# Optimization experiments

Measured on AMD Instinct MI355X. Metric: run time of the kernel, lower is better.

Reference implementation:

```python
import jax, jax.numpy as jnp
import numpy as np
import math

B, C, H, W, M = 8, 256, 128, 128, 7
EPS = 1e-08


def setup_inputs() -> dict:
    key = jax.random.key(0)
    ks = jax.random.split(key, 7)
    x_high = jax.random.normal(ks[0], (B, C, H // 2, W // 2), jnp.float32)
    x_low = jax.random.normal(ks[1], (B, C, H, W), jnp.float32)
    w1 = jax.random.normal(ks[2], (32, M * M), jnp.float32) / np.sqrt(M * M)
    b1 = jnp.zeros((32,), jnp.float32)
    w2 = jax.random.normal(ks[3], (3, 32), jnp.float32) / np.sqrt(32)
    b2 = jnp.zeros((3,), jnp.float32)
    refine_w = jax.random.normal(ks[4], (C, C), jnp.float32) / np.sqrt(C)
    return {"x_high": x_high, "x_low": x_low, "w1": w1, "b1": b1,
            "w2": w2, "b2": b2, "refine_w": refine_w}


def _anisotropic_kernel(params):
    # params: (B,3) -> normalized Gaussian kernels (B, m, m)
    theta = jnp.arctan2(params[:, 0], params[:, 1]) / 2.0 + math.pi / 2.0
    lam1 = jnp.exp(params[:, 2])
    lam2 = 1.0 / (lam1 + EPS)
    coords = jnp.arange(M, dtype=jnp.float32) - (M // 2)  # -3..3
    yy = coords[:, None]  # (m,1) varies along rows (torch meshgrid 'ij')
    xx = coords[None, :]  # (1,m)
    cos_t = jnp.cos(theta)[:, None, None]
    sin_t = jnp.sin(theta)[:, None, None]
    x_rot = xx * cos_t + yy * sin_t          # (B,m,m)
    y_rot = -xx * sin_t + yy * cos_t
    l1 = lam1[:, None, None]
    l2 = lam2[:, None, None]
    k = jnp.exp(-(x_rot ** 2 / (2.0 * l1 ** 2) + y_rot ** 2 / (2.0 * l2 ** 2)))
    return k / (jnp.sum(k, axis=(1, 2), keepdims=True) + EPS)


def _depthwise(x, kern):
    # x: (B,C,H,W), kern: (B,m,m) -> per-sample depthwise conv, kernel shared across C
    k = jnp.repeat(kern, C, axis=0)[:, None, :, :]  # (B*C,1,m,m)
    pad = M // 2
    y = jax.lax.conv_general_dilated(
        x.reshape(1, B * C, H, W), k, (1, 1), [(pad, pad), (pad, pad)],
        dimension_numbers=("NCHW", "OIHW", "NCHW"), feature_group_count=B * C)
    return y.reshape(B, C, H, W)


def reference(x_high, x_low, w1, b1, w2, b2, refine_w):
    # bilinear upsample (align_corners=False == half-pixel, matches jax.image.resize)
    x_high_up = jax.image.resize(x_high, (B, C, H, W), method="bilinear")

    x_f = jnp.fft.fftshift(jnp.fft.fft2(x_low, norm="ortho"), axes=(-2, -1))
    real, imag = jnp.real(x_f), jnp.imag(x_f)
    mag = jnp.abs(x_f)
    mag_weighted = jnp.mean(mag, axis=1, keepdims=True)  # (B,1,H,W)
    h0, w0 = H // 2 - M // 2, W // 2 - M // 2
    mag_center = mag_weighted[:, :, h0:h0 + M, w0:w0 + M]  # (B,1,m,m)

    # param_net: Flatten -> Linear -> ReLU -> Linear
    flat = mag_center.reshape(B, M * M)
    h = jax.nn.relu(flat @ w1.T + b1)
    params = h @ w2.T + b2  # (B,3)

    kern = _anisotropic_kernel(params)
    real_f = _depthwise(real, kern)
    imag_f = _depthwise(imag, kern)

    # 1x1 refine conv (bias-free), shared for real and imag parts
    real_f = jnp.einsum("bchw,oc->bohw", real_f, refine_w)
    imag_f = jnp.einsum("bchw,oc->bohw", imag_f, refine_w)

    out_f = jax.lax.complex(real_f, imag_f)
    out_f = jnp.fft.ifftshift(out_f, axes=(-2, -1))
    x_low_enhanced = jnp.real(jnp.fft.ifft2(out_f, norm="ortho"))
    return x_low_enhanced + x_high_up
```

## Files before the change

### kernel.cpp

```cpp
#include <hip/hip_runtime.h>

typedef __attribute__((ext_vector_type(8))) short bf16x8;
typedef __attribute__((ext_vector_type(4))) float f32x4;
typedef __attribute__((ext_vector_type(4))) int   i32x4;

#define PI_F 3.14159265358979323846f
#define C128 0.0490873852123405f
#define INV_SQRT128 0.0883883476483184f
#define INV128 0.0078125f

#define NB 8
#define NC 256
#define NH 128
#define NW 128
#define IMG 16384
#define NIMG 2048
#define XST 130

#define GH_STRIDE 3200
#define AB_STRIDE 3072

__device__ __forceinline__ unsigned short f2bf(float f){
  unsigned int u = __float_as_uint(f);
  u += 0x7FFFu + ((u >> 16) & 1u);
  return (unsigned short)(u >> 16);
}
__device__ __forceinline__ float bf2f(unsigned short u){
  return __uint_as_float(((unsigned int)u) << 16);
}

__device__ __constant__ int c_pcnt[6] = {1,2,3,3,2,1};
__device__ __constant__ int c_pdp0[6] = {6,5,4,0,0,0};

#define COS1 0.9987954562051724f
#define SIN1 0.0490676743274180f
#define K1CH (2.0f*COS1)

__global__ void __launch_bounds__(256) K1(const float* __restrict__ xlow,
                                          float* __restrict__ GH){
  __shared__ unsigned short xs[128*XST];
  __shared__ float Hlo[4][2][128];
  __shared__ float Hhi[4][2][128];
  __shared__ float Gg [4][2][128];
  __shared__ float twc[128], tws[128];

  const int tid = threadIdx.x;
  const int img = blockIdx.x;
  float* ghb = GH + (size_t)img*GH_STRIDE;

  if (tid < 128){
    float s,c; __sincosf((float)tid*C128, &s, &c);
    twc[tid]=c; tws[tid]=s;
  }
  {
    const float4* xp = (const float4*)(xlow + (size_t)img*IMG);
    #pragma unroll
    for (int k=0; k<16; ++k){
      int e4 = k*256 + tid;
      float4 v = xp[e4];
      int px = e4*4;
      int r = px >> 7, c = px & 127;
      unsigned int pw0 = (unsigned int)f2bf(v.x) | ((unsigned int)f2bf(v.y) << 16);
      unsigned int pw1 = (unsigned int)f2bf(v.z) | ((unsigned int)f2bf(v.w) << 16);
      *(unsigned int*)(&xs[r*XST + c    ]) = pw0;
      *(unsigned int*)(&xs[r*XST + c + 2]) = pw1;
    }
  }
  __syncthreads();

  float A0e=0.f, A0o=0.f;
  float Ce1=0.f,Se1=0.f,Co1=0.f,So1=0.f;
  float Ce2=0.f,Se2=0.f,Co2=0.f,So2=0.f;
  float Ce3=0.f,Se3=0.f,Co3=0.f,So3=0.f;

  if (tid < 128){
    const int r = tid;
    const unsigned short* xr = &xs[r*XST];
    float cp = 1.f, sp = 0.f;
    float cn = COS1, sn = SIN1;
    #pragma unroll 4
    for (int j=0; j<64; ++j){
      unsigned int pk = *(const unsigned int*)(&xr[2*j]);
      float xe = __uint_as_float(pk << 16);
      float xo = __uint_as_float(pk & 0xffff0000u);
      {
        float t2 = cp + cp;
        float c2 = fmaf(t2, cp, -1.f);
        float s2 = t2 * sp;
        float c3 = fmaf(t2, c2, -cp);
        float s3 = fmaf(t2, s2, -sp);
        A0e += xe;
        Ce1 = fmaf(xe, cp, Ce1); Se1 = fmaf(xe, sp, Se1);
        Ce2 = fmaf(xe, c2, Ce2); Se2 = fmaf(xe, s2, Se2);
        Ce3 = fmaf(xe, c3, Ce3); Se3 = fmaf(xe, s3, Se3);
      }
      {
        float t2 = cn + cn;
        float c2 = fmaf(t2, cn, -1.f);
        float s2 = t2 * sn;
        float c3 = fmaf(t2, c2, -cn);
        float s3 = fmaf(t2, s2, -sn);
        A0o += xo;
        Co1 = fmaf(xo, cn, Co1); So1 = fmaf(xo, sn, So1);
        Co2 = fmaf(xo, c2, Co2); So2 = fmaf(xo, s2, So2);
        Co3 = fmaf(xo, c3, Co3); So3 = fmaf(xo, s3, So3);
      }
      float cpn = fmaf(K1CH, cn, -cp);
      float spn = fmaf(K1CH, sn, -sp);
      float cnn = fmaf(K1CH, cpn, -cn);
      float snn = fmaf(K1CH, spn, -sn);
      cp = cpn; sp = spn; cn = cnn; sn = snn;
    }
    Hlo[0][0][r]=A0e+A0o;  Hlo[0][1][r]=0.f;
    Hlo[1][0][r]=Ce1+Co1;  Hlo[1][1][r]=-(Se1+So1);
    Hlo[2][0][r]=Ce2+Co2;  Hlo[2][1][r]=-(Se2+So2);
    Hlo[3][0][r]=Ce3+Co3;  Hlo[3][1][r]=-(Se3+So3);
    Hhi[0][0][r]=Ce3-Co3;  Hhi[0][1][r]=Se3-So3;
    Hhi[1][0][r]=Ce2-Co2;  Hhi[1][1][r]=Se2-So2;
    Hhi[2][0][r]=Ce1-Co1;  Hhi[2][1][r]=Se1-So1;
    Hhi[3][0][r]=A0e-A0o;  Hhi[3][1][r]=0.f;
  } else {
    const int c = tid - 128;
    float cp = 1.f, sp = 0.f;
    float cn = COS1, sn = SIN1;
    #pragma unroll 4
    for (int j=0; j<64; ++j){
      float xe = bf2f(xs[(2*j  )*XST + c]);
      float xo = bf2f(xs[(2*j+1)*XST + c]);
      {
        float t2 = cp + cp;
        float c2 = fmaf(t2, cp, -1.f);
        float s2 = t2 * sp;
        float c3 = fmaf(t2, c2, -cp);
        float s3 = fmaf(t2, s2, -sp);
        A0e += xe;
        Ce1 = fmaf(xe, cp, Ce1); Se1 = fmaf(xe, sp, Se1);
        Ce2 = fmaf(xe, c2, Ce2); Se2 = fmaf(xe, s2, Se2);
        Ce3 = fmaf(xe, c3, Ce3); Se3 = fmaf(xe, s3, Se3);
      }
      {
        float t2 = cn + cn;
        float c2 = fmaf(t2, cn, -1.f);
        float s2 = t2 * sn;
        float c3 = fmaf(t2, c2, -cn);
        float s3 = fmaf(t2, s2, -sn);
        A0o += xo;
        Co1 = fmaf(xo, cn, Co1); So1 = fmaf(xo, sn, So1);
        Co2 = fmaf(xo, c2, Co2); So2 = fmaf(xo, s2, So2);
        Co3 = fmaf(xo, c3, Co3); So3 = fmaf(xo, s3, So3);
      }
      float cpn = fmaf(K1CH, cn, -cp);
      float spn = fmaf(K1CH, sn, -sp);
      float cnn = fmaf(K1CH, cpn, -cn);
      float snn = fmaf(K1CH, spn, -sn);
      cp = cpn; sp = spn; cn = cnn; sn = snn;
    }
    Gg[0][0][c]=Ce3-Co3;  Gg[0][1][c]=Se3-So3;
    Gg[1][0][c]=Ce2-Co2;  Gg[1][1][c]=Se2-So2;
    Gg[2][0][c]=Ce1-Co1;  Gg[2][1][c]=Se1-So1;
    Gg[3][0][c]=A0e-A0o;  Gg[3][1][c]=0.f;
  }
  __syncthreads();

  #pragma unroll
  for (int k=0;k<6;++k){
    int idx = k*256 + tid;
    int w = idx >> 8, reim = (idx >> 7) & 1, c = idx & 127;
    float sg = reim ? -1.f : 1.f;
    float vG, vH;
    if (w < 4){ vG = Gg[w][reim][c];  vH = Hhi[w][reim][c]; }
    else if (w == 4){ vG = sg*Gg[2][reim][c]; vH = sg*Hhi[2][reim][c]; }
    else { vG = sg*Gg[1][reim][c]; vH = sg*Hhi[1][reim][c]; }
    ghb[idx]        = vG * INV_SQRT128;
    ghb[1536 + idx] = vH * INV_SQRT128;
  }
  if (tid < 36){
    int wi = tid/6, zi = tid%6;
    int z = 61 + zi;
    float fR=0.f, fI=0.f;
    for (int c=0;c<128;++c){
      float gR, gI;
      if (wi < 4){ gR = Gg[wi][0][c]; gI = Gg[wi][1][c]; }
      else if (wi == 4){ gR = Gg[2][0][c]; gI = -Gg[2][1][c]; }
      else { gR = Gg[1][0][c]; gI = -Gg[1][1][c]; }
      int m = (z*c) & 127;
      float tc = twc[m], ts = tws[m];
      fR += gR*tc + gI*ts;
      fI += gI*tc - gR*ts;
    }
    ghb[3072 + tid*2]     = fR * INV128;
    ghb[3072 + tid*2 + 1] = fI * INV128;
  }
  if (tid >= 64 && tid < 113){
    int i = tid - 64;
    int u = i/7 - 3, v = i%7 - 3;
    int va = v < 0 ? -v : v;
    float vsg = v < 0 ? -1.f : 1.f;
    float fR=0.f, fI=0.f;
    for (int r=0;r<128;++r){
      float hR = Hlo[va][0][r], hI = vsg*Hlo[va][1][r];
      int m = ((u*r) % 128 + 128) & 127;
      float tc = twc[m], ts = tws[m];
      fR += hR*tc + hI*ts;
      fI += hI*tc - hR*ts;
    }
    fR *= INV128; fI *= INV128;
    ghb[3144 + i] = sqrtf(fR*fR + fI*fI);
  }
}

__global__ void __launch_bounds__(64) K_mlp(const float* __restrict__ GH,
                                            const float* __restrict__ w1,
                                            const float* __restrict__ b1,
                                            const float* __restrict__ w2,
                                            const float* __restrict__ b2,
                                            float* __restrict__ kern){
  __shared__ float flat[49];
  __shared__ float hh[32];
  const int b = blockIdx.x, tid = threadIdx.x;
  if (tid < 49){
    float s = 0.f;
    for (int c=0; c<256; ++c)
      s += GH[(size_t)(b*256 + c)*GH_STRIDE + 3144 + tid];
    flat[tid] = s * (1.0f/256.0f);
  }
  __syncthreads();
  if (tid < 32){
    float s = b1[tid];
    for (int i=0; i<49; ++i) s += flat[i]*w1[tid*49+i];
    hh[tid] = fmaxf(s, 0.f);
  }
  __syncthreads();
  if (tid == 0){
    float p[3];
    #pragma unroll
    for (int k=0; k<3; ++k){
      float s = b2[k];
      for (int j=0; j<32; ++j) s += hh[j]*w2[k*32+j];
      p[k] = s;
    }
    float theta = atan2f(p[0], p[1])*0.5f + 1.57079632679489662f;
    float ct = cosf(theta), st = sinf(theta);
    float l1 = expf(p[2]);
    float l2 = 1.0f/(l1 + 1e-8f);
    float inv1 = 1.0f/(2.0f*l1*l1);
    float inv2 = 1.0f/(2.0f*l2*l2);
    float sum = 0.f;
    for (int i=0; i<7; ++i) for (int j=0; j<7; ++j){
      float yy = (float)(i-3), xx = (float)(j-3);
      float xr =  xx*ct + yy*st;
      float yr = -xx*st + yy*ct;
      sum += expf(-(xr*xr*inv1 + yr*yr*inv2));
    }
    float inv = 1.0f/(sum + 1e-8f);
    for (int i=0; i<7; ++i) for (int j=0; j<7; ++j){
      float yy = (float)(i-3), xx = (float)(j-3);
      float xr =  xx*ct + yy*st;
      float yr = -xx*st + yy*ct;
      kern[b*49 + i*7 + j] = expf(-(xr*xr*inv1 + yr*yr*inv2)) * inv;
    }
  }
}

__global__ void __launch_bounds__(256) K3(const float* __restrict__ kern,
                                          float* __restrict__ KL,
                                          float* __restrict__ W){
  __shared__ float twc[128], tws[128], kl[49];
  __shared__ float kapl[7][2][128];
  const int b = blockIdx.x, tid = threadIdx.x;
  if (tid < 128){
    float s,c; __sincosf((float)tid*C128, &s, &c);
    twc[tid]=c; tws[tid]=s;
  }
  if (tid < 49) kl[tid] = kern[b*49 + tid];
  __syncthreads();
  if (tid < 128){
    const int c = tid;
    float* klb = KL + (size_t)b*3584;
    #pragma unroll
    for (int dp=0; dp<7; ++dp){
      float kR=0.f, kI=0.f;
      #pragma unroll
      for (int dq=0; dq<7; ++dq){
        int m = (((dq-3)*c) % 128 + 128) & 127;
        float kv = kl[dp*7+dq];
        kR += kv*twc[m]; kI -= kv*tws[m];
      }
      klb[(dp*2  )*128 + c] = kR;
      klb[(dp*2+1)*128 + c] = kI;
      kapl[dp][0][c] = kR; kapl[dp][1][c] = kI;
    }
    const int r = tid;
    #pragma unroll
    for (int dq=0; dq<7; ++dq){
      float lR=0.f, lI=0.f;
      #pragma unroll
      for (int dp=0; dp<7; ++dp){
        int m = (((dp-3)*r) % 128 + 128) & 127;
        float kv = kl[dp*7+dq];
        lR += kv*twc[m]; lI -= kv*tws[m];
      }
      klb[1792 + (dq*2  )*128 + r] = lR;
      klb[1792 + (dq*2+1)*128 + r] = lI;
    }
  }
  __syncthreads();
  for (int k=0;k<64;++k){
    int px = k*256 + tid;
    int r = px >> 7, c = px & 127;
    float w = 0.f;
    #pragma unroll
    for (int dp=0; dp<7; ++dp){
      int m = (((dp-3)*r) % 128 + 128) & 127;
      w += twc[m]*kapl[dp][0][c] + tws[m]*kapl[dp][1][c];
    }
    W[(size_t)b*IMG + px] = w;
  }
}

__global__ void __launch_bounds__(128) K_tab(const float* __restrict__ GH,
                                             const float* __restrict__ KL,
                                             const float* __restrict__ kern,
                                             float* __restrict__ AB){
  __shared__ float dRe[36], dIm[36], kl[49];
  const int tid = threadIdx.x;
  const int img = blockIdx.x, b = img >> 8;
  const float* ghb = GH + (size_t)img*GH_STRIDE;
  const float* klb = KL + (size_t)b*3584;
  float* abb = AB + (size_t)img*AB_STRIDE;

  if (tid < 49) kl[tid] = kern[b*49 + tid];
  __syncthreads();
  if (tid < 36){
    int si = tid/6, ti = tid%6;
    float dR=0.f, dI=0.f;
    for (int j=0; j<c_pcnt[si]; ++j){
      int dp = c_pdp0[si] + j;
      int wi = (si-3) + dp;
      for (int l=0; l<c_pcnt[ti]; ++l){
        int dq = c_pdp0[ti] + l;
        int zi = (ti-3) + dq;
        float kv = kl[dp*7+dq];
        dR += kv * ghb[3072 + (wi*6+zi)*2];
        dI += kv * ghb[3072 + (wi*6+zi)*2 + 1];
      }
    }
    dRe[tid] = dR; dIm[tid] = dI;
  }
  __syncthreads();

  const int c = tid;
  float s1,c1; __sincosf((float)c*C128, &s1, &c1);
  float c2 = c1*c1 - s1*s1, s2 = 2.f*c1*s1;
  float c3 = c1*c2 - s1*s2, s3 = s1*c2 + c1*s2;
  float ct[6] = {c3,c2,c1,1.f,c1,c2};
  float st[6] = {-s3,-s2,-s1,0.f,s1,s2};
  float sgnc = (c & 1) ? -1.f : 1.f;

  float gr[6], gi[6], kr[7], ki[7];
  #pragma unroll
  for (int w=0;w<6;++w){ gr[w]=ghb[(w*2)*128+c]; gi[w]=ghb[(w*2+1)*128+c]; }
  #pragma unroll
  for (int dp=0;dp<7;++dp){ kr[dp]=klb[(dp*2)*128+c]; ki[dp]=klb[(dp*2+1)*128+c]; }

  #pragma unroll
  for (int si=0; si<6; ++si){
    float dR=0.f, dI=0.f;
    for (int j=0; j<c_pcnt[si]; ++j){
      int dp = c_pdp0[si] + j;
      int w = (si-3) + dp;
      dR += kr[dp]*gr[w] - ki[dp]*gi[w];
      dI += kr[dp]*gi[w] + ki[dp]*gr[w];
    }
    float corrR=0.f, corrI=0.f;
    #pragma unroll
    for (int ti=0; ti<6; ++ti){
      float DR = dRe[si*6+ti], DI = dIm[si*6+ti];
      corrR += DR*ct[ti] - DI*st[ti];
      corrI += DR*st[ti] + DI*ct[ti];
    }
    abb[(si*2  )*128 + c] = INV_SQRT128*dR - INV128*sgnc*corrR;
    abb[(si*2+1)*128 + c] = INV_SQRT128*dI - INV128*sgnc*corrI;
  }

  const int r = tid;
  float hr[6], hi_[6], lr[7], li[7];
  #pragma unroll
  for (int z=0;z<6;++z){ hr[z]=ghb[1536+(z*2)*128+r]; hi_[z]=ghb[1536+(z*2+1)*128+r]; }
  #pragma unroll
  for (int dq=0;dq<7;++dq){ lr[dq]=klb[1792+(dq*2)*128+r]; li[dq]=klb[1792+(dq*2+1)*128+r]; }
  #pragma unroll
  for (int ti=0; ti<6; ++ti){
    float bR=0.f, bI=0.f;
    for (int l=0; l<c_pcnt[ti]; ++l){
      int dq = c_pdp0[ti] + l;
      int z = (ti-3) + dq;
      bR += lr[dq]*hr[z] - li[dq]*hi_[z];
      bI += lr[dq]*hi_[z] + li[dq]*hr[z];
    }
    abb[1536 + r*12 + ti*2]     = INV_SQRT128*bR;
    abb[1536 + r*12 + ti*2 + 1] = INV_SQRT128*bI;
  }
}

__global__ void __launch_bounds__(256) K4(const float* __restrict__ xlow,
                                          const float* __restrict__ W,
                                          const float* __restrict__ AB,
                                          unsigned short* __restrict__ filt){
  const int tid = threadIdx.x;
  const int img = blockIdx.x, b = img >> 8;
  const int c0 = (tid & 63)*2, grp = tid >> 6;
  const float* abb = AB + (size_t)img*AB_STRIDE;
  const float* xim = xlow + (size_t)img*IMG;
  const float* Wb  = W + (size_t)b*IMG;
  unsigned short* fim = filt + (size_t)img*IMG;

  float ar[2][6], ai[2][6], ctc[2][6], stc[2][6];
  #pragma unroll
  for (int col=0; col<2; ++col){
    int c = c0 + col;
    #pragma unroll
    for (int si=0;si<6;++si){ ar[col][si]=abb[(si*2)*128+c]; ai[col][si]=abb[(si*2+1)*128+c]; }
    float s1,c1; __sincosf((float)c*C128, &s1, &c1);
    float c2 = c1*c1 - s1*s1, s2 = 2.f*c1*s1;
    float c3 = c1*c2 - s1*s2, s3 = s1*c2 + c1*s2;
    ctc[col][0]=c3; ctc[col][1]=c2; ctc[col][2]=c1; ctc[col][3]=1.f; ctc[col][4]=c1; ctc[col][5]=c2;
    stc[col][0]=-s3; stc[col][1]=-s2; stc[col][2]=-s1; stc[col][3]=0.f; stc[col][4]=s1; stc[col][5]=s2;
  }

  for (int k=0;k<32;++k){
    int ru = __builtin_amdgcn_readfirstlane(grp*32 + k);
    const float* brow = abb + 1536 + ru*12;
    float4 b0 = *(const float4*)(brow);
    float4 b1 = *(const float4*)(brow+4);
    float4 b2 = *(const float4*)(brow+8);
    float rs1,rc1; __sincosf((float)ru*C128, &rs1, &rc1);
    float rc2 = rc1*rc1 - rs1*rs1, rs2 = 2.f*rc1*rs1;
    float rc3 = rc1*rc2 - rs1*rs2, rs3 = rs1*rc2 + rc1*rs2;
    float rcs[6] = {rc3,rc2,rc1,1.f,rc1,rc2};
    float rss[6] = {-rs3,-rs2,-rs1,0.f,rs1,rs2};

    float ER0 = 0.f, ER1 = 0.f;
    #pragma unroll
    for (int si=0;si<6;++si){
      ER0 += rcs[si]*ar[0][si] - rss[si]*ai[0][si];
      ER1 += rcs[si]*ar[1][si] - rss[si]*ai[1][si];
    }
    float rsg = (ru & 1) ? -1.f : 1.f;
    ER0 *= rsg; ER1 *= rsg;

    float bRv[6] = {b0.x, b0.z, b1.x, b1.z, b2.x, b2.z};
    float bIv[6] = {b0.y, b0.w, b1.y, b1.w, b2.y, b2.w};
    float EC0 = 0.f, EC1 = 0.f;
    #pragma unroll
    for (int ti=0;ti<6;++ti){
      EC0 += ctc[0][ti]*bRv[ti] - stc[0][ti]*bIv[ti];
      EC1 += ctc[1][ti]*bRv[ti] - stc[1][ti]*bIv[ti];
    }
    int px = ru*128 + c0;
    float2 xv = *(const float2*)(&xim[px]);
    float2 wv = *(const float2*)(&Wb[px]);
    float v0 = xv.x*wv.x - ER0 - EC0;
    float v1 = xv.y*wv.y - ER1 + EC1;
    unsigned int pack = ((unsigned int)f2bf(v1) << 16) | (unsigned int)f2bf(v0);
    *(unsigned int*)(&fim[px]) = pack;
  }
}

__global__ void __launch_bounds__(256) K_w(const float* __restrict__ rw,
                                           unsigned short* __restrict__ rwbf){
  int i = blockIdx.x*256 + threadIdx.x;
  rwbf[i] = f2bf(rw[i]);
}

__global__ void __launch_bounds__(256) K_up(const float* __restrict__ xhigh,
                                            unsigned short* __restrict__ up){
  __shared__ float xs[64*68];
  const int tid = threadIdx.x;
  const int img = blockIdx.x;
  const float* src = xhigh + (size_t)img*4096;
  unsigned short* dst = up + (size_t)img*IMG;

  #pragma unroll
  for (int p=0; p<4; ++p){
    int t = p*256 + tid;
    float4 v = ((const float4*)src)[t];
    int r = t >> 4, k = t & 15;
    *(float4*)(&xs[r*68 + k*4]) = v;
  }
  __syncthreads();

  for (int k=0; k<32; ++k){
    int pr = k*256 + tid;
    int y = pr >> 6, x0 = (pr & 63)*2;
    float fy = 0.5f*(float)y - 0.25f;
    int iyf = (int)floorf(fy);
    float ty = fy - (float)iyf;
    int iy0 = iyf < 0 ? 0 : iyf;
    int iy1 = (iyf+1) > 63 ? 63 : (iyf+1);
    float wy1 = ty, wy0 = 1.0f - ty;
    const float* r0 = &xs[iy0*68];
    const float* r1 = &xs[iy1*68];

    float outv[2];
    #pragma unroll
    for (int e=0; e<2; ++e){
      int x = x0 + e;
      float fx = 0.5f*(float)x - 0.25f;
      int ixf = (int)floorf(fx);
      float tx = fx - (float)ixf;
      int ix0 = ixf < 0 ? 0 : ixf;
      int ix1 = (ixf+1) > 63 ? 63 : (ixf+1);
      float wx1 = tx, wx0 = 1.0f - tx;
      outv[e] = wy0*(wx0*r0[ix0] + wx1*r0[ix1])
              + wy1*(wx0*r1[ix0] + wx1*r1[ix1]);
    }
    unsigned int pack = ((unsigned int)f2bf(outv[1]) << 16) | (unsigned int)f2bf(outv[0]);
    *(unsigned int*)(&dst[y*NW + x0]) = pack;
  }
}

__global__ void __launch_bounds__(256) K_trans(const unsigned short* __restrict__ in,
                                               unsigned short* __restrict__ outT){
  __shared__ unsigned short tile[64*68];
  const int p0 = blockIdx.x * 64;
  const int c0 = blockIdx.y * 64;
  const int b  = blockIdx.z;
  const int tid = threadIdx.x;
  const int lo = tid >> 4;
  const int q4 = (tid & 15) * 4;

  #pragma unroll
  for (int pass=0; pass<4; ++pass){
    int cc = lo + pass*16;
    ushort4 v = *(const ushort4*)(&in[((size_t)b*NC + c0 + cc)*IMG + p0 + q4]);
    tile[(q4+0)*68 + cc] = v.x;
    tile[(q4+1)*68 + cc] = v.y;
    tile[(q4+2)*68 + cc] = v.z;
    tile[(q4+3)*68 + cc] = v.w;
  }
  __syncthreads();
  #pragma unroll
  for (int pass=0; pass<4; ++pass){
    int pp = lo + pass*16;
    ushort4 v = *(const ushort4*)(&tile[pp*68 + q4]);
    *(ushort4*)(&outT[((size_t)b*IMG + p0 + pp)*NC + c0 + q4]) = v;
  }
}

__global__ void __launch_bounds__(256) K_gemm(const unsigned short* __restrict__ rwbf,
                                              const unsigned short* __restrict__ filtT,
                                              const unsigned short* __restrict__ up,
                                              float* __restrict__ out){
  __shared__ unsigned short At[2][128*32];
  __shared__ unsigned short Bt[2][128*32];
  const int tid = threadIdx.x, lane = tid & 63, wv = tid >> 6;
  const int wr = wv >> 1, wc = wv & 1;
  const int xg = blockIdx.x;
  const int g16 = xg >> 4, i16 = xg & 15;
  const int ot = i16 >> 3, pt = (g16 << 3) | (i16 & 7);
  const int b = blockIdx.z;
  const int p0 = pt*128, o0 = ot*128;

  f32x4 acc[4][4];
  #pragma unroll
  for (int m=0;m<4;++m)
    #pragma unroll
    for (int n=0;n<4;++n){ f32x4 z = {0.f,0.f,0.f,0.f}; acc[m][n] = z; }

  const int row  = tid >> 2;
  const int koff = (tid & 3) * 8;
  const unsigned short* aP0 = &rwbf[(size_t)(o0+row   )*256 + koff];
  const unsigned short* aP1 = &rwbf[(size_t)(o0+row+64)*256 + koff];
  const unsigned short* bP0 = &filtT[((size_t)b*IMG + p0+row   )*256 + koff];
  const unsigned short* bP1 = &filtT[((size_t)b*IMG + p0+row+64)*256 + koff];

  i32x4 av0 = *(const i32x4*)(aP0);
  i32x4 av1 = *(const i32x4*)(aP1);
  i32x4 bv0 = *(const i32x4*)(bP0);
  i32x4 bv1 = *(const i32x4*)(bP1);
  *(i32x4*)(&At[0][ row     *32 + koff]) = av0;
  *(i32x4*)(&At[0][(row+64) *32 + koff]) = av1;
  *(i32x4*)(&Bt[0][ row     *32 + koff]) = bv0;
  *(i32x4*)(&Bt[0][(row+64) *32 + koff]) = bv1;
  __syncthreads();

  const int g = lane >> 4, r16 = lane & 15;
  for (int ks=0; ks<8; ++ks){
    const int cur = ks & 1;
    if (ks < 7){
      const int k0 = (ks+1)*32;
      av0 = *(const i32x4*)(aP0 + k0);
      av1 = *(const i32x4*)(aP1 + k0);
      bv0 = *(const i32x4*)(bP0 + k0);
      bv1 = *(const i32x4*)(bP1 + k0);
    }
    bf16x8 af[4], bfr[4];
    #pragma unroll
    for (int m=0;m<4;++m) af[m]  = *(const bf16x8*)(&At[cur][(wr*64 + m*16 + r16)*32 + g*8]);
    #pragma unroll
    for (int n=0;n<4;++n) bfr[n] = *(const bf16x8*)(&Bt[cur][(wc*64 + n*16 + r16)*32 + g*8]);
    #pragma unroll
    for (int m=0;m<4;++m)
      #pragma unroll
      for (int n=0;n<4;++n)
        acc[m][n] = __builtin_amdgcn_mfma_f32_16x16x32_bf16(af[m], bfr[n], acc[m][n], 0, 0, 0);
    if (ks < 7){
      const int nxt = cur ^ 1;
      *(i32x4*)(&At[nxt][ row     *32 + koff]) = av0;
      *(i32x4*)(&At[nxt][(row+64) *32 + koff]) = av1;
      *(i32x4*)(&Bt[nxt][ row     *32 + koff]) = bv0;
      *(i32x4*)(&Bt[nxt][(row+64) *32 + koff]) = bv1;
      __syncthreads();
    }
  }

  const int y = pt;
  #pragma unroll
  for (int m=0;m<4;++m){
    #pragma unroll
    for (int j=0;j<4;++j){
      int o = o0 + wr*64 + m*16 + g*4 + j;
      size_t base = (size_t)(b*NC + o)*IMG + (size_t)y*NW;
      #pragma unroll
      for (int n=0;n<4;++n){
        int xcol = wc*64 + n*16 + r16;
        float upv = bf2f(up[base + xcol]);
        out[base + xcol] = acc[m][n][j] + upv;
      }
    }
  }
}

extern "C" void kernel_launch(void* const* d_in, const int* in_sizes, int n_in,
                              void* d_out, int out_size, void* d_ws, size_t ws_size,
                              hipStream_t stream){
  (void)in_sizes; (void)n_in; (void)out_size; (void)ws_size;
  const float* xhigh = (const float*)d_in[0];
  const float* xlow  = (const float*)d_in[1];
  const float* w1    = (const float*)d_in[2];
  const float* b1    = (const float*)d_in[3];
  const float* w2    = (const float*)d_in[4];
  const float* b2    = (const float*)d_in[5];
  const float* rw    = (const float*)d_in[6];

  char* ws = (char*)d_ws;
  unsigned short* filt  = (unsigned short*)(ws);
  unsigned short* filtT = (unsigned short*)(ws + 67108864);
  float* GH   = (float*)(ws + 134217728);
  float* AB   = (float*)(ws + 160432128);
  float* kern = (float*)(ws + 185597952);
  float* KL   = (float*)(ws + 185602048);
  float* Wf   = (float*)(ws + 185716736);
  unsigned short* rwbf = (unsigned short*)(ws + 186241024);
  unsigned short* up   = filt;

  K1   <<<NIMG, 256, 0, stream>>>(xlow, GH);
  K_mlp<<<NB,   64,  0, stream>>>(GH, w1, b1, w2, b2, kern);
  K3   <<<NB,   256, 0, stream>>>(kern, KL, Wf);
  K_w  <<<256,  256, 0, stream>>>(rw, rwbf);
  K_tab<<<NIMG, 128, 0, stream>>>(GH, KL, kern, AB);
  K4   <<<NIMG, 256, 0, stream>>>(xlow, Wf, AB, filt);
  K_trans<<<dim3(256, 4, NB), 256, 0, stream>>>(filt, filtT);
  K_up <<<NIMG, 256, 0, stream>>>(xhigh, up);
  K_gemm <<<dim3(256, 1, NB), 256, 0, stream>>>(rwbf, filtT, up, (float*)d_out);
}
```

Baseline: 314.1 us.

## Split K1 partial DFT sums across 512 threads with shared-memory reduction

```diff
diff --git a/kernel.cpp b/kernel.cpp
--- a/kernel.cpp
+++ b/kernel.cpp
@@ -15,7 +15,6 @@
 #define NW 128
 #define IMG 16384
 #define NIMG 2048
-#define XST 130
 
 #define GH_STRIDE 3200
 #define AB_STRIDE 3072
@@ -36,176 +35,190 @@
 #define SIN1 0.0490676743274180f
 #define K1CH (2.0f*COS1)
 
-__global__ void __launch_bounds__(256) K1(const float* __restrict__ xlow,
-                                          float* __restrict__ GH){
-  __shared__ unsigned short xs[128*XST];
-  __shared__ float Hlo[4][2][128];
-  __shared__ float Hhi[4][2][128];
-  __shared__ float Gg [4][2][128];
-  __shared__ float twc[128], tws[128];
-
+#define SM_GG   8320
+#define SM_HLR  9344
+#define SM_HLI  9856
+#define SM_SCRG 1920
+
+__global__ void __launch_bounds__(512, 8) K1(const float* __restrict__ xlow,
+                                             float* __restrict__ GH){
+  __shared__ float smem[10240];
+  unsigned short* xs = (unsigned short*)smem;
   const int tid = threadIdx.x;
   const int img = blockIdx.x;
   float* ghb = GH + (size_t)img*GH_STRIDE;
 
-  if (tid < 128){
-    float s,c; __sincosf((float)tid*C128, &s, &c);
-    twc[tid]=c; tws[tid]=s;
-  }
   {
     const float4* xp = (const float4*)(xlow + (size_t)img*IMG);
     #pragma unroll
-    for (int k=0; k<16; ++k){
-      int e4 = k*256 + tid;
+    for (int k=0; k<8; ++k){
+      int e4 = k*512 + tid;
       float4 v = xp[e4];
-      int px = e4*4;
-      int r = px >> 7, c = px & 127;
+      int r = e4 >> 5, c = (e4 & 31)*4;
       unsigned int pw0 = (unsigned int)f2bf(v.x) | ((unsigned int)f2bf(v.y) << 16);
       unsigned int pw1 = (unsigned int)f2bf(v.z) | ((unsigned int)f2bf(v.w) << 16);
-      *(unsigned int*)(&xs[r*XST + c    ]) = pw0;
-      *(unsigned int*)(&xs[r*XST + c + 2]) = pw1;
-    }
-  }
-  __syncthreads();
-
-  float A0e=0.f, A0o=0.f;
-  float Ce1=0.f,Se1=0.f,Co1=0.f,So1=0.f;
-  float Ce2=0.f,Se2=0.f,Co2=0.f,So2=0.f;
-  float Ce3=0.f,Se3=0.f,Co3=0.f,So3=0.f;
-
-  if (tid < 128){
-    const int r = tid;
-    const unsigned short* xr = &xs[r*XST];
-    float cp = 1.f, sp = 0.f;
-    float cn = COS1, sn = SIN1;
-    #pragma unroll 4
-    for (int j=0; j<64; ++j){
-      unsigned int pk = *(const unsigned int*)(&xr[2*j]);
-      float xe = __uint_as_float(pk << 16);
-      float xo = __uint_as_float(pk & 0xffff0000u);
-      {
-        float t2 = cp + cp;
-        float c2 = fmaf(t2, cp, -1.f);
-        float s2 = t2 * sp;
-        float c3 = fmaf(t2, c2, -cp);
-        float s3 = fmaf(t2, s2, -sp);
-        A0e += xe;
-        Ce1 = fmaf(xe, cp, Ce1); Se1 = fmaf(xe, sp, Se1);
-        Ce2 = fmaf(xe, c2, Ce2); Se2 = fmaf(xe, s2, Se2);
-        Ce3 = fmaf(xe, c3, Ce3); Se3 = fmaf(xe, s3, Se3);
+      *(unsigned int*)(&xs[r*130 + c    ]) = pw0;
+      *(unsigned int*)(&xs[r*130 + c + 2]) = pw1;
+    }
+  }
+  __syncthreads();
+
+  float acc[14];
+  #pragma unroll
+  for (int i=0;i<14;++i) acc[i]=0.f;
+
+  const int isRow = (tid < 256);
+  const int lid  = isRow ? tid : (tid-256);
+  const int idx  = lid & 127;
+  const int half = lid >> 7;
+
+  {
+    const float sg0 = half ? -1.f : 1.f;
+    float cp = sg0, sp = 0.f;
+    float cn = sg0*COS1, sn = sg0*SIN1;
+
+#define K1_ACCUM(xv, cc, ss)                                   \
+    {                                                          \
+      float t2 = cc + cc;                                      \
+      float c2 = fmaf(t2, cc, -1.f);                           \
+      float s2 = t2 * ss;                                      \
+      float c3 = fmaf(t2, c2, -cc);                            \
+      float s3 = fmaf(t2, s2, -ss);                            \
+      acc[0 + PARITY] += xv;                                   \
+      acc[2 + PARITY*2]  = fmaf(xv, cc, acc[2 + PARITY*2]);    \
+      acc[3 + PARITY*2]  = fmaf(xv, ss, acc[3 + PARITY*2]);    \
+      acc[6 + PARITY*2]  = fmaf(xv, c2, acc[6 + PARITY*2]);    \
+      acc[7 + PARITY*2]  = fmaf(xv, s2, acc[7 + PARITY*2]);    \
+      acc[10 + PARITY*2] = fmaf(xv, c3, acc[10 + PARITY*2]);   \
+      acc[11 + PARITY*2] = fmaf(xv, s3, acc[11 + PARITY*2]);   \
+    }
+
+    if (isRow){
+      const unsigned short* xr = &xs[idx*130 + half*64];
+      #pragma unroll 4
+      for (int j=0; j<32; ++j){
+        unsigned int pk = *(const unsigned int*)(&xr[2*j]);
+        float xe = __uint_as_float(pk << 16);
+        float xo = __uint_as_float(pk & 0xffff0000u);
+#define PARITY 0
+        K1_ACCUM(xe, cp, sp)
+#undef PARITY
+#define PARITY 1
+        K1_ACCUM(xo, cn, sn)
+#undef PARITY
+        float cpn = fmaf(K1CH, cn, -cp);
+        float spn = fmaf(K1CH, sn, -sp);
+        float cnn = fmaf(K1CH, cpn, -cn);
+        float snn = fmaf(K1CH, spn, -sn);
+        cp = cpn; sp = spn; cn = cnn; sn = snn;
       }
-      {
-        float t2 = cn + cn;
-        float c2 = fmaf(t2, cn, -1.f);
-        float s2 = t2 * sn;
-        float c3 = fmaf(t2, c2, -cn);
-        float s3 = fmaf(t2, s2, -sn);
-        A0o += xo;
-        Co1 = fmaf(xo, cn, Co1); So1 = fmaf(xo, sn, So1);
-        Co2 = fmaf(xo, c2, Co2); So2 = fmaf(xo, s2, So2);
-        Co3 = fmaf(xo, c3, Co3); So3 = fmaf(xo, s3, So3);
+    } else {
+      const unsigned short* xc = &xs[half*64*130 + idx];
+      #pragma unroll 4
+      for (int j=0; j<32; ++j){
+        float xe = bf2f(xc[(2*j  )*130]);
+        float xo = bf2f(xc[(2*j+1)*130]);
+#define PARITY 0
+        K1_ACCUM(xe, cp, sp)
+#undef PARITY
+#define PARITY 1
+        K1_ACCUM(xo, cn, sn)
+#undef PARITY
+        float cpn = fmaf(K1CH, cn, -cp);
+        float spn = fmaf(K1CH, sn, -sp);
+        float cnn = fmaf(K1CH, cpn, -cn);
+        float snn = fmaf(K1CH, spn, -sn);
+        cp = cpn; sp = spn; cn = cnn; sn = snn;
       }
-      float cpn = fmaf(K1CH, cn, -cp);
-      float spn = fmaf(K1CH, sn, -sp);
-      float cnn = fmaf(K1CH, cpn, -cn);
-      float snn = fmaf(K1CH, spn, -sn);
-      cp = cpn; sp = spn; cn = cnn; sn = snn;
-    }
-    Hlo[0][0][r]=A0e+A0o;  Hlo[0][1][r]=0.f;
-    Hlo[1][0][r]=Ce1+Co1;  Hlo[1][1][r]=-(Se1+So1);
-    Hlo[2][0][r]=Ce2+Co2;  Hlo[2][1][r]=-(Se2+So2);
-    Hlo[3][0][r]=Ce3+Co3;  Hlo[3][1][r]=-(Se3+So3);
-    Hhi[0][0][r]=Ce3-Co3;  Hhi[0][1][r]=Se3-So3;
-    Hhi[1][0][r]=Ce2-Co2;  Hhi[1][1][r]=Se2-So2;
-    Hhi[2][0][r]=Ce1-Co1;  Hhi[2][1][r]=Se1-So1;
-    Hhi[3][0][r]=A0e-A0o;  Hhi[3][1][r]=0.f;
-  } else {
-    const int c = tid - 128;
-    float cp = 1.f, sp = 0.f;
-    float cn = COS1, sn = SIN1;
-    #pragma unroll 4
-    for (int j=0; j<64; ++j){
-      float xe = bf2f(xs[(2*j  )*XST + c]);
-      float xo = bf2f(xs[(2*j+1)*XST + c]);
-      {
-        float t2 = cp + cp;
-        float c2 = fmaf(t2, cp, -1.f);
-        float s2 = t2 * sp;
-        float c3 = fmaf(t2, c2, -cp);
-        float s3 = fmaf(t2, s2, -sp);
-        A0e += xe;
-        Ce1 = fmaf(xe, cp, Ce1); Se1 = fmaf(xe, sp, Se1);
-        Ce2 = fmaf(xe, c2, Ce2); Se2 = fmaf(xe, s2, Se2);
-        Ce3 = fmaf(xe, c3, Ce3); Se3 = fmaf(xe, s3, Se3);
-      }
-      {
-        float t2 = cn + cn;
-        float c2 = fmaf(t2, cn, -1.f);
-        float s2 = t2 * sn;
-        float c3 = fmaf(t2, c2, -cn);
-        float s3 = fmaf(t2, s2, -sn);
-        A0o += xo;
-        Co1 = fmaf(xo, cn, Co1); So1 = fmaf(xo, sn, So1);
-        Co2 = fmaf(xo, c2, Co2); So2 = fmaf(xo, s2, So2);
-        Co3 = fmaf(xo, c3, Co3); So3 = fmaf(xo, s3, So3);
-      }
-      float cpn = fmaf(K1CH, cn, -cp);
-      float spn = fmaf(K1CH, sn, -sp);
-      float cnn = fmaf(K1CH, cpn, -cn);
-      float snn = fmaf(K1CH, spn, -sn);
-      cp = cpn; sp = spn; cn = cnn; sn = snn;
-    }
-    Gg[0][0][c]=Ce3-Co3;  Gg[0][1][c]=Se3-So3;
-    Gg[1][0][c]=Ce2-Co2;  Gg[1][1][c]=Se2-So2;
-    Gg[2][0][c]=Ce1-Co1;  Gg[2][1][c]=Se1-So1;
-    Gg[3][0][c]=A0e-A0o;  Gg[3][1][c]=0.f;
-  }
-  __syncthreads();
-
-  #pragma unroll
-  for (int k=0;k<6;++k){
-    int idx = k*256 + tid;
-    int w = idx >> 8, reim = (idx >> 7) & 1, c = idx & 127;
-    float sg = reim ? -1.f : 1.f;
-    float vG, vH;
-    if (w < 4){ vG = Gg[w][reim][c];  vH = Hhi[w][reim][c]; }
-    else if (w == 4){ vG = sg*Gg[2][reim][c]; vH = sg*Hhi[2][reim][c]; }
-    else { vG = sg*Gg[1][reim][c]; vH = sg*Hhi[1][reim][c]; }
-    ghb[idx]        = vG * INV_SQRT128;
-    ghb[1536 + idx] = vH * INV_SQRT128;
-  }
-  if (tid < 36){
-    int wi = tid/6, zi = tid%6;
-    int z = 61 + zi;
+    }
+#undef K1_ACCUM
+  }
+  __syncthreads();
+
+  const int scrbase = (isRow ? 0 : SM_SCRG) + idx*15;
+  if (half){
+    #pragma unroll
+    for (int i=0;i<14;++i) smem[scrbase+i] = acc[i];
+  }
+  __syncthreads();
+  if (!half){
+    #pragma unroll
+    for (int i=0;i<14;++i) acc[i] += smem[scrbase+i];
+    float A0e=acc[0],A0o=acc[1],Ce1=acc[2],Se1=acc[3],Co1=acc[4],So1=acc[5],
+          Ce2=acc[6],Se2=acc[7],Co2=acc[8],So2=acc[9],
+          Ce3=acc[10],Se3=acc[11],Co3=acc[12],So3=acc[13];
+    float d0  = A0e-A0o;
+    float dc1 = Ce1-Co1, ds1 = Se1-So1;
+    float dc2 = Ce2-Co2, ds2 = Se2-So2;
+    float dc3 = Ce3-Co3, ds3 = Se3-So3;
+    float* gp = ghb + (isRow ? 1536 : 0);
+    const int k = idx;
+    gp[(0*2+0)*128+k] = dc3*INV_SQRT128;  gp[(0*2+1)*128+k] =  ds3*INV_SQRT128;
+    gp[(1*2+0)*128+k] = dc2*INV_SQRT128;  gp[(1*2+1)*128+k] =  ds2*INV_SQRT128;
+    gp[(2*2+0)*128+k] = dc1*INV_SQRT128;  gp[(2*2+1)*128+k] =  ds1*INV_SQRT128;
+    gp[(3*2+0)*128+k] = d0 *INV_SQRT128;  gp[(3*2+1)*128+k] =  0.f;
+    gp[(4*2+0)*128+k] = dc1*INV_SQRT128;  gp[(4*2+1)*128+k] = -ds1*INV_SQRT128;
+    gp[(5*2+0)*128+k] = dc2*INV_SQRT128;  gp[(5*2+1)*128+k] = -ds2*INV_SQRT128;
+    if (isRow){
+      smem[SM_HLR + 0*128 + k] = A0e+A0o;
+      smem[SM_HLR + 1*128 + k] = Ce1+Co1;
+      smem[SM_HLR + 2*128 + k] = Ce2+Co2;
+      smem[SM_HLR + 3*128 + k] = Ce3+Co3;
+      smem[SM_HLI + 0*128 + k] = -(Se1+So1);
+      smem[SM_HLI + 1*128 + k] = -(Se2+So2);
+      smem[SM_HLI + 2*128 + k] = -(Se3+So3);
+    } else {
+      smem[SM_GG + (0*2+0)*128 + k] = dc3;  smem[SM_GG + (0*2+1)*128 + k] = ds3;
+      smem[SM_GG + (1*2+0)*128 + k] = dc2;  smem[SM_GG + (1*2+1)*128 + k] = ds2;
+      smem[SM_GG + (2*2+0)*128 + k] = dc1;  smem[SM_GG + (2*2+1)*128 + k] = ds1;
+      smem[SM_GG + (3*2+0)*128 + k] = d0;   smem[SM_GG + (3*2+1)*128 + k] = 0.f;
+    }
+  }
+  __syncthreads();
+
+  if (tid < 144){
+    int out = tid >> 2, chunk = tid & 3;
+    int wi = out/6, zi = out%6, z = 61+zi;
+    int wsrc = (wi<4) ? wi : (wi==4 ? 2 : 1);
+    float isg = (wi<4) ? 1.f : -1.f;
     float fR=0.f, fI=0.f;
-    for (int c=0;c<128;++c){
-      float gR, gI;
-      if (wi < 4){ gR = Gg[wi][0][c]; gI = Gg[wi][1][c]; }
-      else if (wi == 4){ gR = Gg[2][0][c]; gI = -Gg[2][1][c]; }
-      else { gR = Gg[1][0][c]; gI = -Gg[1][1][c]; }
+    const int cEnd = chunk*32 + 32;
+    for (int c=chunk*32; c<cEnd; ++c){
+      float gR = smem[SM_GG + (wsrc*2  )*128 + c];
+      float gI = isg*smem[SM_GG + (wsrc*2+1)*128 + c];
       int m = (z*c) & 127;
-      float tc = twc[m], ts = tws[m];
+      float ts, tc; __sincosf((float)m*C128, &ts, &tc);
       fR += gR*tc + gI*ts;
       fI += gI*tc - gR*ts;
     }
-    ghb[3072 + tid*2]     = fR * INV128;
-    ghb[3072 + tid*2 + 1] = fI * INV128;
-  }
-  if (tid >= 64 && tid < 113){
-    int i = tid - 64;
+    fR += __shfl_xor(fR,1); fI += __shfl_xor(fI,1);
+    fR += __shfl_xor(fR,2); fI += __shfl_xor(fI,2);
+    if (chunk==0){
+      ghb[3072 + out*2]     = fR * INV128;
+      ghb[3072 + out*2 + 1] = fI * INV128;
+    }
+  }
+  if (tid >= 256 && tid < 452){
+    int i = (tid-256) >> 2, chunk = (tid-256) & 3;
     int u = i/7 - 3, v = i%7 - 3;
     int va = v < 0 ? -v : v;
     float vsg = v < 0 ? -1.f : 1.f;
     float fR=0.f, fI=0.f;
-    for (int r=0;r<128;++r){
-      float hR = Hlo[va][0][r], hI = vsg*Hlo[va][1][r];
+    const int rEnd = chunk*32 + 32;
+    for (int r=chunk*32; r<rEnd; ++r){
+      float hR = smem[SM_HLR + va*128 + r];
+      float hI = (va==0) ? 0.f : vsg*smem[SM_HLI + (va-1)*128 + r];
       int m = ((u*r) % 128 + 128) & 127;
-      float tc = twc[m], ts = tws[m];
+      float ts, tc; __sincosf((float)m*C128, &ts, &tc);
       fR += hR*tc + hI*ts;
       fI += hI*tc - hR*ts;
     }
-    fR *= INV128; fI *= INV128;
-    ghb[3144 + i] = sqrtf(fR*fR + fI*fI);
+    fR += __shfl_xor(fR,1); fI += __shfl_xor(fI,1);
+    fR += __shfl_xor(fR,2); fI += __shfl_xor(fI,2);
+    if (chunk==0){
+      fR *= INV128; fI *= INV128;
+      ghb[3144 + i] = sqrtf(fR*fR + fI*fI);
+    }
   }
 }
 
@@ -655,7 +668,7 @@
   unsigned short* rwbf = (unsigned short*)(ws + 186241024);
   unsigned short* up   = filt;
 
-  K1   <<<NIMG, 256, 0, stream>>>(xlow, GH);
+  K1   <<<NIMG, 512, 0, stream>>>(xlow, GH);
   K_mlp<<<NB,   64,  0, stream>>>(GH, w1, b1, w2, b2, kern);
   K3   <<<NB,   256, 0, stream>>>(kern, KL, Wf);
   K_w  <<<256,  256, 0, stream>>>(rw, rwbf);
```

Measured after the change: 293.7 us. -6.5%, faster.
